# Performance work log

Hardware: AMD Instinct MI355X
Metric: run time of the kernel (lower is better)

Reference implementation:

```python
import jax, jax.numpy as jnp
import numpy as np

IN_FEATURES = 1024
OUT_FEATURES = 512
TAU_U = 20.0
DT = 1.0


def setup_inputs() -> dict:
    key = jax.random.key(0)
    k_x, k_w = jax.random.split(key)
    B, T = 32, 1024
    x = jax.random.normal(k_x, (B, T, IN_FEATURES), dtype=jnp.float32)
    # uniform(-sqrt(1/in), sqrt(1/in)) as in reset_parameters
    bound = float(np.sqrt(1.0 / IN_FEATURES))
    weight = jax.random.uniform(k_w, (OUT_FEATURES, IN_FEATURES), dtype=jnp.float32,
                                minval=-bound, maxval=bound)
    bias = jnp.zeros((OUT_FEATURES,), dtype=jnp.float32)
    # fixed tau trainer: decay = exp(-dt / tau), tau fixed at 20
    decay_u = jnp.full((OUT_FEATURES,), float(np.exp(-DT / TAU_U)), dtype=jnp.float32)
    return {"x": x, "weight": weight, "bias": bias, "decay_u": decay_u}


def reference(x, weight, bias, decay_u):
    # x: [B, T, in] -> current: [B, T, out] (one big GEMM instead of T small ones)
    current = jnp.einsum("bti,oi->bto", x, weight) + bias
    B = x.shape[0]
    u0 = jnp.zeros((B, OUT_FEATURES), dtype=x.dtype)

    drive = (1.0 - decay_u) * current          # [B, T, out]
    drive_t = jnp.swapaxes(drive, 0, 1)        # [T, B, out] for scan

    def step(u_tm1, d_t):
        u_t = decay_u * u_tm1 + d_t
        return u_t, u_t

    _, outs_t = jax.lax.scan(step, u0, drive_t)  # [T, B, out]
    outputs = jnp.swapaxes(outs_t, 0, 1)          # [B, T, out]
    # states: stack([u0, u1, ..., uT], dim=1).unsqueeze(0) -> [1, B, T+1, out]
    states = jnp.concatenate([u0[:, None, :], outputs], axis=1)[None]
    return outputs, states
```

## Files before the change

### kernel.cpp

```cpp
#include <hip/hip_runtime.h>
#include <hip/hip_bf16.h>
#include <stdint.h>

#define BATCH 32
#define SEQT  1024
#define INF   1024
#define OUTF  512
#define MROWS (BATCH * SEQT)

typedef __attribute__((ext_vector_type(8))) short short8;
typedef __attribute__((ext_vector_type(4))) float f32x4;

__device__ __forceinline__ short f2bf(float f) {
    return (short)__builtin_bit_cast(unsigned short, __float2bfloat16(f));
}

__device__ __forceinline__ void gll16(const float* g, float* l) {
    __builtin_amdgcn_global_load_lds(
        (const __attribute__((address_space(1))) unsigned int*)g,
        (__attribute__((address_space(3))) unsigned int*)l, 16, 0, 0);
}

__global__ __launch_bounds__(512, 2) void gemm_bf16_kernel(
    const float* __restrict__ X, const float* __restrict__ W,
    const float* __restrict__ bias, __hip_bfloat16* __restrict__ C) {
    __shared__ float lds_f[32768];

    const int tid = threadIdx.x;
    const int bid = blockIdx.x;
    const int xcd = bid & 7;
    const int ii  = bid >> 3;
    const int mt  = (xcd << 4) + (ii >> 1);
    const int nt  = ii & 1;
    const int m0 = mt << 8;
    const int o0 = nt << 8;

    const int wv   = tid >> 6;
    const int lane = tid & 63;
    const int wr = wv >> 1;
    const int wc = wv & 1;
    const int r0 = lane & 15;
    const int lg = lane >> 4;

    const float* srcA[4];
    const float* srcB[4];
    int dstf[4];
#pragma unroll
    for (int j = 0; j < 4; ++j) {
        const int g = (j << 9) + tid;
        const int r = g >> 3;
        const int s = (g & 7) ^ (r & 7);
        dstf[j] = g << 2;
        srcA[j] = X + (size_t)(m0 + r) * INF + (s << 2);
        srcB[j] = W + (size_t)(o0 + r) * INF + (s << 2);
    }

#define STAGE(BUF, KB)                                                       \
    {                                                                        \
        float* ba_ = &lds_f[(BUF) << 14];                                    \
        float* bb_ = ba_ + 8192;                                             \
        _Pragma("unroll")                                                    \
        for (int j = 0; j < 4; ++j) gll16(srcA[j] + (KB), &ba_[dstf[j]]);    \
        _Pragma("unroll")                                                    \
        for (int j = 0; j < 4; ++j) gll16(srcB[j] + (KB), &bb_[dstf[j]]);    \
    }

    f32x4 acc[4][8] = {};

    STAGE(0, 0)
    __syncthreads();

    for (int kt = 0; kt < 32; ++kt) {
        if (kt < 31) STAGE((kt + 1) & 1, (kt + 1) << 5);
        const float* ba = &lds_f[(kt & 1) << 14];
        const float* bb = ba + 8192;

        short8 av[4], bv[8];
#pragma unroll
        for (int mi = 0; mi < 4; ++mi) {
            const int r  = (wr << 6) + (mi << 4) + r0;
            const int s0 = (lg << 1) ^ (r & 7);
            const f32x4 u0 = *(const f32x4*)&ba[(r << 5) + (s0 << 2)];
            const f32x4 u1 = *(const f32x4*)&ba[(r << 5) + ((s0 ^ 1) << 2)];
            short8 h;
#pragma unroll
            for (int j = 0; j < 4; ++j) { h[j] = f2bf(u0[j]); h[4 + j] = f2bf(u1[j]); }
            av[mi] = h;
        }
#pragma unroll
        for (int ni = 0; ni < 8; ++ni) {
            const int r  = (wc << 7) + (ni << 4) + r0;
            const int s0 = (lg << 1) ^ (r & 7);
            const f32x4 u0 = *(const f32x4*)&bb[(r << 5) + (s0 << 2)];
            const f32x4 u1 = *(const f32x4*)&bb[(r << 5) + ((s0 ^ 1) << 2)];
            short8 h;
#pragma unroll
            for (int j = 0; j < 4; ++j) { h[j] = f2bf(u0[j]); h[4 + j] = f2bf(u1[j]); }
            bv[ni] = h;
        }
#pragma unroll
        for (int mi = 0; mi < 4; ++mi)
#pragma unroll
            for (int ni = 0; ni < 8; ++ni)
                acc[mi][ni] = __builtin_amdgcn_mfma_f32_16x16x32_bf16(
                    av[mi], bv[ni], acc[mi][ni], 0, 0, 0);

        __syncthreads();
    }

    short* cs = (short*)lds_f;
#pragma unroll
    for (int pass = 0; pass < 2; ++pass) {
        if ((wr >> 1) == pass) {
#pragma unroll
            for (int ni = 0; ni < 8; ++ni) {
                const int col = (wc << 7) + (ni << 4) + r0;
                const float bbv = bias[o0 + col];
#pragma unroll
                for (int mi = 0; mi < 4; ++mi) {
                    const int lr = ((wr & 1) << 6) + (mi << 4) + (lg << 2);
#pragma unroll
                    for (int j = 0; j < 4; ++j)
                        cs[(lr + j) * 264 + col] = f2bf(acc[mi][ni][j] + bbv);
                }
            }
        }
        __syncthreads();
        short* cg = (short*)C;
#pragma unroll
        for (int sw = 0; sw < 8; ++sw) {
            const int row = (sw << 4) + (tid >> 5);
            const int gr  = tid & 31;
            short8 v = *(const short8*)&cs[row * 264 + (gr << 3)];
            *(short8*)&cg[(size_t)(m0 + (pass << 7) + row) * OUTF + o0 + (gr << 3)] = v;
        }
        if (pass == 0) __syncthreads();
    }
#undef STAGE
}

template <bool WRITE_OUT>
__global__ __launch_bounds__(256) void scan_kernel(
    const __hip_bfloat16* __restrict__ cur, float* __restrict__ outp,
    float* __restrict__ states, const float* __restrict__ decay) {
    const int gid = blockIdx.x * 256 + threadIdx.x;
    const int o   = gid & 511;
    const int seg = (gid >> 9) & 7;
    const int b   = gid >> 12;

    const float d   = decay[o];
    const float omd = 1.0f - d;
    const __hip_bfloat16* c = cur + (size_t)b * (SEQT * OUTF) + o;
    float* sp = states + (size_t)b * ((SEQT + 1) * OUTF) + o;

    if (seg == 0) sp[0] = 0.0f;

    float u = 0.0f;
    const int t0 = seg << 7;
    const int tw = (seg == 0) ? 0 : (t0 - 128);
    for (int t = tw; t < t0; t += 8) {
        float r[8];
#pragma unroll
        for (int j = 0; j < 8; ++j) r[j] = __bfloat162float(c[(size_t)(t + j) * OUTF]);
#pragma unroll
        for (int j = 0; j < 8; ++j) u = fmaf(d, u, omd * r[j]);
    }
    float* op = outp + (size_t)b * (SEQT * OUTF) + o;
    for (int t = t0; t < t0 + 128; t += 8) {
        float r[8];
#pragma unroll
        for (int j = 0; j < 8; ++j) r[j] = __bfloat162float(c[(size_t)(t + j) * OUTF]);
        float uu[8];
#pragma unroll
        for (int j = 0; j < 8; ++j) { u = fmaf(d, u, omd * r[j]); uu[j] = u; }
#pragma unroll
        for (int j = 0; j < 8; ++j) sp[(size_t)(t + 1 + j) * OUTF] = uu[j];
        if (WRITE_OUT) {
#pragma unroll
            for (int j = 0; j < 8; ++j) op[(size_t)(t + j) * OUTF] = uu[j];
        }
    }
}

__global__ __launch_bounds__(256) void copy_out_kernel(
    float* __restrict__ outp, const float* __restrict__ states) {
    const size_t total = (size_t)MROWS * OUTF / 4;
    size_t i = (size_t)blockIdx.x * blockDim.x + threadIdx.x;
    const size_t stride = (size_t)gridDim.x * blockDim.x;
    for (; i < total; i += stride) {
        const size_t flat = i * 4;
        const size_t o  = flat & 511;
        const size_t bt = flat >> 9;
        const size_t b  = bt >> 10;
        const size_t t  = bt & 1023;
        *(f32x4*)&outp[flat] =
            *(const f32x4*)&states[(b * (SEQT + 1) + t + 1) * OUTF + o];
    }
}

extern "C" void kernel_launch(void* const* d_in, const int* in_sizes, int n_in,
                              void* d_out, int out_size, void* d_ws, size_t ws_size,
                              hipStream_t stream) {
    const float* x     = (const float*)d_in[0];
    const float* w     = (const float*)d_in[1];
    const float* bias  = (const float*)d_in[2];
    const float* decay = (const float*)d_in[3];

    float* outp   = (float*)d_out;
    float* states = outp + (size_t)MROWS * OUTF;

    const size_t cur_bytes = (size_t)MROWS * OUTF * sizeof(__hip_bfloat16);
    const bool use_ws = (ws_size >= cur_bytes);
    __hip_bfloat16* cur = use_ws ? (__hip_bfloat16*)d_ws : (__hip_bfloat16*)outp;

    gemm_bf16_kernel<<<dim3(256), dim3(512), 0, stream>>>(x, w, bias, cur);

    if (use_ws) {
        scan_kernel<true><<<dim3(512), dim3(256), 0, stream>>>(cur, outp, states, decay);
    } else {
        scan_kernel<false><<<dim3(512), dim3(256), 0, stream>>>(cur, nullptr, states, decay);
        copy_out_kernel<<<dim3(2048), dim3(256), 0, stream>>>(outp, states);
    }
}
```

Before: 106.3 us.

## Convert GEMM tiles to bf16 before LDS via register-staged prefetch

Replaces direct global-to-LDS fp32 loads with global loads into registers. Each value is converted to bf16 once and written into a swizzled bf16 LDS layout after the MFMAs of the current k-step. This halves LDS footprint and read traffic and removes the per-wave redundant fp32-to-bf16 conversion on fragment reads. It also adds setprio around the MFMA block and sched barriers. The cost is more VGPRs for staged loads and conversion ALU work sitting between compute and the barrier.

```diff
diff --git a/kernel.cpp b/kernel.cpp
--- a/kernel.cpp
+++ b/kernel.cpp
@@ -15,16 +15,16 @@
     return (short)__builtin_bit_cast(unsigned short, __float2bfloat16(f));
 }
 
-__device__ __forceinline__ void gll16(const float* g, float* l) {
-    __builtin_amdgcn_global_load_lds(
-        (const __attribute__((address_space(1))) unsigned int*)g,
-        (__attribute__((address_space(3))) unsigned int*)l, 16, 0, 0);
+__device__ __forceinline__ int swzoff(int r, int s) {
+    const int line = r >> 1;
+    const int sl = (s | ((r & 1) << 2)) ^ (line & 7);
+    return (line << 6) + (sl << 3);
 }
 
 __global__ __launch_bounds__(512, 2) void gemm_bf16_kernel(
     const float* __restrict__ X, const float* __restrict__ W,
     const float* __restrict__ bias, __hip_bfloat16* __restrict__ C) {
-    __shared__ float lds_f[32768];
+    __shared__ short lds_s[33792];
 
     const int tid = threadIdx.x;
     const int bid = blockIdx.x;
@@ -42,73 +42,85 @@
     const int r0 = lane & 15;
     const int lg = lane >> 4;
 
-    const float* srcA[4];
-    const float* srcB[4];
-    int dstf[4];
-#pragma unroll
-    for (int j = 0; j < 4; ++j) {
+    int gdst[2];
+    const float* gA[2];
+    const float* gB[2];
+#pragma unroll
+    for (int j = 0; j < 2; ++j) {
         const int g = (j << 9) + tid;
-        const int r = g >> 3;
-        const int s = (g & 7) ^ (r & 7);
-        dstf[j] = g << 2;
-        srcA[j] = X + (size_t)(m0 + r) * INF + (s << 2);
-        srcB[j] = W + (size_t)(o0 + r) * INF + (s << 2);
-    }
-
-#define STAGE(BUF, KB)                                                       \
+        const int r = g >> 2;
+        const int s = g & 3;
+        gdst[j] = swzoff(r, s);
+        gA[j] = X + (size_t)(m0 + r) * INF + (s << 3);
+        gB[j] = W + (size_t)(o0 + r) * INF + (s << 3);
+    }
+
+    f32x4 sA[2][2], sB[2][2];
+
+#define ISSUE_LOADS(KB)                                                      \
+    _Pragma("unroll")                                                        \
+    for (int j = 0; j < 2; ++j) {                                            \
+        sA[j][0] = *(const f32x4*)(gA[j] + (KB));                            \
+        sA[j][1] = *(const f32x4*)(gA[j] + (KB) + 4);                        \
+        sB[j][0] = *(const f32x4*)(gB[j] + (KB));                            \
+        sB[j][1] = *(const f32x4*)(gB[j] + (KB) + 4);                        \
+    }
+
+#define CVT_WRITE(BUF)                                                       \
     {                                                                        \
-        float* ba_ = &lds_f[(BUF) << 14];                                    \
-        float* bb_ = ba_ + 8192;                                             \
+        short* la_ = &lds_s[(BUF) << 14];                                    \
+        short* lb_ = la_ + 8192;                                             \
         _Pragma("unroll")                                                    \
-        for (int j = 0; j < 4; ++j) gll16(srcA[j] + (KB), &ba_[dstf[j]]);    \
-        _Pragma("unroll")                                                    \
-        for (int j = 0; j < 4; ++j) gll16(srcB[j] + (KB), &bb_[dstf[j]]);    \
+        for (int j = 0; j < 2; ++j) {                                        \
+            short8 ha, hb;                                                   \
+            _Pragma("unroll")                                                \
+            for (int q = 0; q < 4; ++q) {                                    \
+                ha[q] = f2bf(sA[j][0][q]); ha[4 + q] = f2bf(sA[j][1][q]);    \
+                hb[q] = f2bf(sB[j][0][q]); hb[4 + q] = f2bf(sB[j][1][q]);    \
+            }                                                                \
+            *(short8*)&la_[gdst[j]] = ha;                                    \
+            *(short8*)&lb_[gdst[j]] = hb;                                    \
+        }                                                                    \
     }
 
     f32x4 acc[4][8] = {};
 
-    STAGE(0, 0)
+    ISSUE_LOADS(0)
+    CVT_WRITE(0)
     __syncthreads();
 
     for (int kt = 0; kt < 32; ++kt) {
-        if (kt < 31) STAGE((kt + 1) & 1, (kt + 1) << 5);
-        const float* ba = &lds_f[(kt & 1) << 14];
-        const float* bb = ba + 8192;
-
+        const int cur = kt & 1;
+        if (kt < 31) { ISSUE_LOADS((kt + 1) << 5) }
+        __builtin_amdgcn_sched_barrier(0);
+
+        const short* la = &lds_s[cur << 14];
+        const short* lb = la + 8192;
         short8 av[4], bv[8];
 #pragma unroll
-        for (int mi = 0; mi < 4; ++mi) {
-            const int r  = (wr << 6) + (mi << 4) + r0;
-            const int s0 = (lg << 1) ^ (r & 7);
-            const f32x4 u0 = *(const f32x4*)&ba[(r << 5) + (s0 << 2)];
-            const f32x4 u1 = *(const f32x4*)&ba[(r << 5) + ((s0 ^ 1) << 2)];
-            short8 h;
-#pragma unroll
-            for (int j = 0; j < 4; ++j) { h[j] = f2bf(u0[j]); h[4 + j] = f2bf(u1[j]); }
-            av[mi] = h;
-        }
-#pragma unroll
-        for (int ni = 0; ni < 8; ++ni) {
-            const int r  = (wc << 7) + (ni << 4) + r0;
-            const int s0 = (lg << 1) ^ (r & 7);
-            const f32x4 u0 = *(const f32x4*)&bb[(r << 5) + (s0 << 2)];
-            const f32x4 u1 = *(const f32x4*)&bb[(r << 5) + ((s0 ^ 1) << 2)];
-            short8 h;
-#pragma unroll
-            for (int j = 0; j < 4; ++j) { h[j] = f2bf(u0[j]); h[4 + j] = f2bf(u1[j]); }
-            bv[ni] = h;
-        }
+        for (int mi = 0; mi < 4; ++mi)
+            av[mi] = *(const short8*)&la[swzoff((wr << 6) + (mi << 4) + r0, lg)];
+#pragma unroll
+        for (int ni = 0; ni < 8; ++ni)
+            bv[ni] = *(const short8*)&lb[swzoff((wc << 7) + (ni << 4) + r0, lg)];
+
+        __builtin_amdgcn_s_setprio(1);
 #pragma unroll
         for (int mi = 0; mi < 4; ++mi)
 #pragma unroll
             for (int ni = 0; ni < 8; ++ni)
                 acc[mi][ni] = __builtin_amdgcn_mfma_f32_16x16x32_bf16(
                     av[mi], bv[ni], acc[mi][ni], 0, 0, 0);
-
+        __builtin_amdgcn_s_setprio(0);
+        __builtin_amdgcn_sched_barrier(0);
+
+        if (kt < 31) { CVT_WRITE(cur ^ 1) }
         __syncthreads();
     }
-
-    short* cs = (short*)lds_f;
+#undef ISSUE_LOADS
+#undef CVT_WRITE
+
+    short* cs = lds_s;
 #pragma unroll
     for (int pass = 0; pass < 2; ++pass) {
         if ((wr >> 1) == pass) {
@@ -136,7 +148,6 @@
         }
         if (pass == 0) __syncthreads();
     }
-#undef STAGE
 }
 
 template <bool WRITE_OUT>
```

Result: no change. 105.2 us (-1.1%).
